# Optimization experiments

Measured on AMD Instinct MI355X. Metric: run time of the kernel, lower is better.

Reference implementation:

```python
import jax, jax.numpy as jnp
import numpy as np
from math import factorial

H = W = 1024
NSC = 4   # n_scales
NOR = 4   # n_orientations
NA = 9


def _grids(h, w):
    # normalized frequency grids, DC at (h//2, w//2) after fftshift
    x = (jnp.arange(w) - w // 2) / (w / 2)
    y = (jnp.arange(h) - h // 2) / (h / 2)
    xr, yr = jnp.meshgrid(x, y, indexing='xy')  # (h, w)
    ang = jnp.arctan2(yr, xr)
    rad = jnp.sqrt(xr * xr + yr * yr)
    rad = rad.at[h // 2, w // 2].set(rad[h // 2, w // 2 - 1])  # avoid log2(0)
    return jnp.log2(rad), ang


def _rc(lr, shift):
    # raised-cosine transition of width 1 (in log2 radius); returns (hi, lo) masks
    t = jnp.clip(lr + shift, 0.0, 1.0)
    return jnp.sin(0.5 * jnp.pi * t), jnp.cos(0.5 * jnp.pi * t)


def _build_pyr(im):
    """Complex steerable pyramid in the frequency domain (downsampled),
    returning (residual highpass, oriented complex bands, residual lowpass,
    unoriented bandpass per scale)."""
    h, w = im.shape
    lr, _ = _grids(h, w)
    hi0m, lo0m = _rc(lr, 1.0)
    imdft = jnp.fft.fftshift(jnp.fft.fft2(im))
    hi0 = jnp.fft.ifft2(jnp.fft.ifftshift(imdft * hi0m)).real
    lodft = imdft * lo0m
    order = NOR - 1
    const = (2.0 ** (2 * order)) * (factorial(order) ** 2) / (NOR * factorial(2 * order))
    bands, unor = [], []
    for s in range(NSC):
        hh, ww = lodft.shape
        lr, ang = _grids(hh, ww)
        him, _ = _rc(lr, 2.0)
        for b in range(NOR):
            th = ang - jnp.pi * b / NOR
            thw = jnp.mod(th + jnp.pi, 2.0 * jnp.pi) - jnp.pi
            am = 2.0 * np.sqrt(const) * (jnp.cos(th) ** order) * (jnp.abs(thw) < jnp.pi / 2)
            bdft = ((-1j) ** order) * lodft * (am * him)
            bands.append(jnp.fft.ifft2(jnp.fft.ifftshift(bdft)))
        unor.append(jnp.fft.ifft2(jnp.fft.ifftshift(lodft * him)).real)
        # downsample lowpass by 2 (crop center of spectrum), apply next lo mask
        lodft = lodft[hh // 4: hh - hh // 4, ww // 4: ww - ww // 4]
        lr2, _ = _grids(hh // 2, ww // 2)
        _, lom = _rc(lr2, 1.0)
        lodft = lodft * lom
    lowpass = jnp.fft.ifft2(jnp.fft.ifftshift(lodft)).real
    return hi0, bands, lowpass, unor


def _autocorr_crop(x, denom, le):
    F = jnp.fft.fft2(x)
    ac = jnp.fft.fftshift(jnp.fft.ifft2(F * jnp.conj(F)).real) / denom
    cx, cy = x.shape[0] // 2, x.shape[1] // 2
    return ac[cx - le: cx + le + 1, cy - le: cy + le + 1]


def _expand(t, f):
    # frequency-domain upsampling by factor f (zero-pad centered spectrum)
    mx, my = t.shape
    T = (f * f) * jnp.fft.fftshift(jnp.fft.fft2(t))
    Te = jnp.zeros((f * mx, f * my), dtype=T.dtype)
    cx, cy = f * mx // 2, f * my // 2
    Te = Te.at[cx - mx // 2: cx + mx // 2, cy - my // 2: cy + my // 2].set(T)
    return jnp.fft.ifft2(jnp.fft.ifftshift(Te))


def _ps_stats(im0):
    S, O, Na = NSC, NOR, NA
    n = im0.size
    mn0, mx0 = jnp.min(im0), jnp.max(im0)
    mean0 = jnp.mean(im0)
    var0 = jnp.sum((im0 - mean0) ** 2) / (n - 1)  # unbiased, like torch.var
    skew0 = jnp.mean((im0 - mean0) ** 3) / var0 ** 1.5
    kurt0 = jnp.mean(jnp.abs(im0 - mean0) ** 4) / var0 ** 2
    statg0 = jnp.stack([mean0, var0, skew0, kurt0, mn0, mx0])

    hi0, bands, lowpass, unor = _build_pyr(im0)
    lowpass = lowpass - jnp.mean(lowpass)
    pyr = [hi0] + bands + [lowpass]
    apyr = [jnp.abs(c) for c in pyr]
    magMeans = jnp.stack([jnp.mean(a) for a in apyr])
    apyr = [a - magMeans[i] for i, a in enumerate(apyr)]

    la = (Na - 1) // 2
    acr = jnp.zeros((Na, Na, S + 1), jnp.float32)
    ace = jnp.zeros((Na, Na, S, O), jnp.float32)
    skew0p = jnp.zeros((S + 1,), jnp.float32)
    kurt0p = jnp.zeros((S + 1,), jnp.float32)

    # ---- lowpass residual: re-filter with height-0 pyramid lowpass (lo0 mask) ----
    ch = lowpass
    le = min(min(ch.shape) // 2 - 1, la)
    lr, _ = _grids(ch.shape[0], ch.shape[1])
    _, lo0m = _rc(lr, 1.0)
    imlp = jnp.fft.ifft2(jnp.fft.ifftshift(jnp.fft.fftshift(jnp.fft.fft2(ch)) * lo0m)).real
    ac = _autocorr_crop(imlp, ch.size, le)
    acr = acr.at[la - le: la + le + 1, la - le: la + le + 1, S].set(ac)
    vari = ac[le, le]
    ok = vari / var0 > 1e-6
    skew0p = skew0p.at[S].set(jnp.where(ok, jnp.mean(imlp ** 3) / vari ** 1.5, 0.0))
    kurt0p = kurt0p.at[S].set(jnp.where(ok, jnp.mean(imlp ** 4) / vari ** 2, 3.0))

    # ---- per-band magnitude autocorr + unoriented band moments ----
    for s in range(S):
        le = la
        for b in range(O):
            chb = apyr[s * O + b + 1]
            le = min(min(chb.shape) // 2 - 1, la)
            ac = _autocorr_crop(chb, chb.size, le)
            ace = ace.at[la - le: la + le + 1, la - le: la + le + 1, s, b].set(ac)
        chu = unor[s]
        # torch stacks (real, zeros): numel doubles, cubic/quartic means halve
        ac = _autocorr_crop(chu, 2 * chu.size, le)
        acr = acr.at[la - le: la + le + 1, la - le: la + le + 1, s].set(ac)
        vari = ac[le, le]
        ok = vari / var0 > 1e-6
        skew0p = skew0p.at[s].set(jnp.where(ok, 0.5 * jnp.mean(chu ** 3) / vari ** 1.5, 0.0))
        kurt0p = kurt0p.at[s].set(jnp.where(ok, 0.5 * jnp.mean(chu ** 4) / vari ** 2, 3.0))

    # ---- cross-orientation / cross-scale correlations ----
    C0 = jnp.zeros((O, O, S + 1), jnp.float32)
    Cx0 = jnp.zeros((O, O, S), jnp.float32)
    Cr0 = jnp.zeros((2 * O, 2 * O, S + 1), jnp.float32)
    Crx0 = jnp.zeros((2 * O, 2 * O, S), jnp.float32)
    for s in range(S):
        csz = pyr[s * O + 1].size
        if s < S - 1:
            pc, rc = [], []
            for b in range(O):
                tmp = _expand(pyr[(s + 1) * O + b + 1], 2) / 4
                r, i = tmp.real, tmp.imag
                mag = jnp.sqrt(r * r + i * i)
                ph = 2.0 * jnp.arctan2(r, i)  # swapped args: faithful to source
                rc.append((mag * jnp.cos(ph), mag * jnp.sin(ph)))
                pc.append(mag)  # |(rt2, it2)| == mag
            parents = jnp.stack([(m - m.mean()).T.ravel() for m in pc], 1)
            rparents = jnp.stack([r.T.ravel() for r, _ in rc] + [i.T.ravel() for _, i in rc], 1)
        else:
            tmp = _expand(lowpass, 2).real / 4
            rparents = jnp.stack([
                tmp.ravel(),
                jnp.roll(tmp, (0, 1), (0, 1)).ravel(),
                jnp.roll(tmp, (0, -1), (0, 1)).ravel(),
                jnp.roll(tmp, (1, 0), (0, 1)).ravel(),
                jnp.roll(tmp, (-1, 0), (0, 1)).ravel()], 1)
            parents = None
        cous = jnp.stack([apyr[s * O + b + 1].T.ravel() for b in range(O)], 1)
        C0 = C0.at[:, :, s].set(cous.T @ cous / csz)
        if parents is not None:
            Cx0 = Cx0.at[:, :, s].set(cous.T @ parents / csz)
        rcous = jnp.stack([pyr[s * O + b + 1].real.T.ravel() for b in range(O)], 1)
        Cr0 = Cr0.at[:O, :O, s].set(rcous.T @ rcous / csz)
        nrp = rparents.shape[1]
        Crx0 = Crx0.at[:O, :nrp, s].set(rcous.T @ rparents / csz)
        if s == S - 1:
            Cr0 = Cr0.at[:nrp, :nrp, S].set(rparents.T @ rparents / (csz / 4))

    vHPR0 = jnp.mean(hi0 ** 2)
    return jnp.concatenate([
        statg0, magMeans, ace.ravel(), skew0p, kurt0p, acr.ravel(),
        C0.ravel(), Cx0.ravel(), Cr0.ravel(), Crx0.ravel(), vHPR0[None]])


def setup_inputs() -> dict:
    key = jax.random.key(0)
    im0 = jax.random.normal(key, (H, W), dtype=jnp.float32)
    return {"im0": im0}


def reference(im0):
    return _ps_stats(im0)
```

## Files before the change

### kernel.cpp

```cpp
#include <hip/hip_runtime.h>

#define PI_F     3.14159265358979323846f
#define TWOPI_F  6.28318530717958647692f
#define HPI_F    1.57079632679489661923f

constexpr int fftT(int N){ return N>=512 ? 256 : (N/2 < 64 ? 64 : N/2); }

#define SL_ACE 340
#define SL_ACR 996
#define SL_ALP 1160
#define SL_TOT 1280
#define REP 8

__device__ __forceinline__ float fcoord(int k, int n){
  int s = k ^ (n>>1);
  return (float)(s - (n>>1)) / (float)(n>>1);
}
__device__ __forceinline__ float lograd(int kr, int kc, int n){
  if (kr==0 && kc==0) return log2f(2.0f/(float)n);
  float x = fcoord(kc,n), y = fcoord(kr,n);
  return 0.5f*log2f(x*x+y*y);
}
__device__ __forceinline__ float rc_sin(float lr, float shift){
  float t = fminf(fmaxf(lr+shift,0.f),1.f); return __sinf(HPI_F*t);
}
__device__ __forceinline__ float rc_cos(float lr, float shift){
  float t = fminf(fmaxf(lr+shift,0.f),1.f); return __cosf(HPI_F*t);
}
__device__ __forceinline__ float cumlo(float lr, int s){
  float cl = rc_cos(lr, 1.f);
  for (int m=1;m<=s;m++) cl *= rc_cos(lr, 1.f-(float)m);
  return cl;
}
__device__ __forceinline__ float bandmask(int kr, int kc, int n, int b){
  float x = fcoord(kc,n), y = fcoord(kr,n);
  float ang = atan2f(y,x);
  float lr = lograd(kr,kc,n);
  float him = rc_sin(lr,2.0f);
  float th = ang - 0.25f*PI_F*(float)b;
  float u = th + PI_F;
  u -= TWOPI_F*floorf(u*(1.0f/TWOPI_F));
  float thw = u - PI_F;
  float c = __cosf(th);
  float am = (fabsf(thw) < HPI_F) ? (1.7888543819998317f*c*c*c) : 0.0f;
  return am*him;
}
__device__ __forceinline__ int lagIdx(int di, int dj){
  if (dj < 0 || (dj==0 && di<0)){ di=-di; dj=-dj; }
  return dj==0 ? 36+di : (dj-1)*9 + (di+4);
}
__device__ __forceinline__ void atomAddD(double* p, double v){
  unsafeAtomicAdd(p, v);
}
template<int NS>
__device__ __forceinline__ void blockAccumN(double* base, const float* vals, float* red){
  const int lane = threadIdx.x & 63, wid = threadIdx.x >> 6;
  const int nw = (int)(blockDim.x >> 6);
  #pragma unroll
  for (int k=0;k<NS;k++){
    float v = vals[k];
    #pragma unroll
    for (int o=32;o>0;o>>=1) v += __shfl_down(v,o);
    if (lane==0) red[k*nw+wid]=v;
  }
  __syncthreads();
  const int rep = (int)((blockIdx.x ^ (blockIdx.y<<1) ^ (blockIdx.z<<2)) & 7) * SL_TOT;
  if ((int)threadIdx.x < NS){
    float s=0.f;
    for (int w2=0;w2<nw;w2++) s += red[(int)threadIdx.x*nw+w2];
    atomAddD(base+rep+(int)threadIdx.x,(double)s);
  }
  __syncthreads();
}

struct ImgD { const float2* src; float2* dst; double* slots; int pre, post, b, ss; float scale; };
struct BArgs { ImgD img[6]; const float* rsrc; const float2* F; const float2* aux; float dirsign; };

#define TWI(k) ((k)+((k)>>4))

template<int N>
__global__ __launch_bounds__(fftT(N)) void k_fftB(BArgs a){
  constexpr int T = fftT(N);
  constexpr int LG = (N==1024)?10:(N==512)?9:(N==256)?8:(N==128)?7:6;
  __shared__ float2 sm[2][N];
  __shared__ float2 tw[N/2 + N/32];
  __shared__ float red[13*4];
  const ImgD d = a.img[blockIdx.y];
  const int row = blockIdx.x, tid = threadIdx.x;
  bool zrow=false;

  for (int k=tid;k<N/2;k+=T){
    float sn,cs; __sincosf(TWOPI_F*(float)k/(float)N,&sn,&cs);
    tw[TWI(k)]=make_float2(cs,sn);
  }

  switch(d.pre){
    case 0: {
      const float2* sp = d.src + (size_t)row*N;
      for (int i=tid;i<N;i+=T) sm[0][i]=sp[i];
    } break;
    case 1: {
      const float* rp = a.rsrc + (size_t)row*N;
      for (int i=tid;i<N;i+=T) sm[0][i]=make_float2(rp[i],0.f);
    } break;
    case 2: {
      const int KC = row + ((row < N/2)? 0 : (1024-N));
      const float2* Fr = a.F + (size_t)KC*1024;
      for (int i=tid;i<N;i+=T){
        int KR = i + ((i < N/2)? 0 : (1024-N));
        float2 v = Fr[KR];
        float lr = lograd(i,row,N);
        float m = cumlo(lr,d.ss)*bandmask(i,row,N,d.b);
        sm[0][i]=make_float2(-v.y*m, v.x*m);
      }
    } break;
    case 3: {
      const int KC = row + ((row < N/2)? 0 : (1024-N));
      const float2* Fr = a.F + (size_t)KC*1024;
      for (int i=tid;i<N;i+=T){
        int KR = i + ((i < N/2)? 0 : (1024-N));
        float2 v = Fr[KR];
        float lr = lograd(i,row,N);
        float m = cumlo(lr,d.ss)*rc_sin(lr,2.f);
        sm[0][i]=make_float2(v.x*m, v.y*m);
      }
    } break;
    case 4: {
      const float2* Fr = a.F + (size_t)row*1024;
      for (int i=tid;i<N;i+=T){
        float2 v = Fr[i];
        float m = rc_sin(lograd(i,row,N),1.f);
        sm[0][i]=make_float2(v.x*m, v.y*m);
      }
    } break;
    case 5: case 6: {
      constexpr int M=N/2, Q=N/4;
      const int fi = (row<Q)? row : (row>=N-Q ? row-M : -1);
      if (fi<0){
        for (int i=tid;i<N;i+=T) sm[0][i]=make_float2(0.f,0.f);
        zrow=true;
      } else {
        const int KC = fi + ((fi < M/2)? 0 : (1024-M));
        const float2* Fr = a.F + (size_t)KC*1024;
        for (int i=tid;i<N;i+=T){
          int fj = (i<Q)? i : (i>=N-Q ? i-M : -1);
          float2 r = make_float2(0.f,0.f);
          if (fj>=0){
            int KR = fj + ((fj < M/2)? 0 : (1024-M));
            float2 v = Fr[KR];
            float lr = lograd(fj,fi,M);
            if (d.pre==5){
              float m = cumlo(lr,d.ss+1)*bandmask(fj,fi,M,d.b);
              r = make_float2(-v.y*m, v.x*m);
            } else {
              if (!(fi==0 && fj==0)){
                float m = cumlo(lr,4);
                r = make_float2(v.x*m, v.y*m);
              }
            }
          }
          sm[0][i]=r;
        }
      }
    } break;
  }

  int cur=0;
  if (!zrow){
    const float ds = a.dirsign;
    for (int ls=0; ls<LG; ++ls){
      const int Ns=1<<ls, sh=LG-1-ls;
      __syncthreads();
      for (int j=tid; j<N/2; j+=T){
        const int m = j & (Ns-1);
        const int base = ((j>>ls)<<(ls+1)) + m;
        float2 va = sm[cur][j];
        float2 vb = sm[cur][j+N/2];
        float2 w = tw[TWI(m<<sh)];
        float wy = ds*w.y;
        float2 bw = make_float2(vb.x*w.x - vb.y*wy, vb.x*wy + vb.y*w.x);
        sm[cur^1][base]    = make_float2(va.x+bw.x, va.y+bw.y);
        sm[cur^1][base+Ns] = make_float2(va.x-bw.x, va.y-bw.y);
      }
      cur ^= 1;
    }
  }
  __syncthreads();

  const float sc = d.scale;
  switch(d.post){
    case 0: {
      float2* dp = d.dst + (size_t)row*N;
      for (int i=tid;i<N;i+=T){ float2 v=sm[cur][i]; dp[i]=make_float2(v.x*sc,v.y*sc); }
    } break;
    case 1: {
      float a1=0.f,a2=0.f;
      for (int i=tid;i<N;i+=T){ float v=sm[cur][i].x*sc; a1+=fabsf(v); a2+=v*v; }
      float vals[2]={a1,a2};
      blockAccumN<2>(d.slots, vals, red);
    } break;
    case 2: {
      float2* dp = d.dst + (size_t)row*N;
      float am=0.f;
      for (int i=tid;i<N;i+=T){
        float2 v=sm[cur][i]; v.x*=sc; v.y*=sc; dp[i]=v;
        am += sqrtf(v.x*v.x+v.y*v.y);
      }
      float vals[1]={am};
      blockAccumN<1>(d.slots, vals, red);
    } break;
    case 3: {
      float2* dp = d.dst + (size_t)row*N;
      float s2=0.f,s3=0.f,s4=0.f;
      for (int i=tid;i<N;i+=T){
        float2 v=sm[cur][i]; v.x*=sc; v.y*=sc; dp[i]=v;
        float x=v.x, x2=x*x; s2+=x2; s3+=x2*x; s4+=x2*x2;
      }
      float vals[3]={s2,s3,s4};
      blockAccumN<3>(d.slots, vals, red);
    } break;
    case 4: {
      const float2* B = a.aux;
      constexpr size_t N2 = (size_t)N*N;
      float acc[13];
      #pragma unroll
      for (int k=0;k<13;k++) acc[k]=0.f;
      for (int i=tid;i<N;i+=T){
        float2 p=sm[cur][i]; p.x*=sc; p.y*=sc;
        float m = sqrtf(p.x*p.x+p.y*p.y);
        float rp=0.f, ip=0.f;
        if (m>0.f){ rp=(p.y*p.y-p.x*p.x)/m; ip=2.f*p.x*p.y/m; }
        size_t pos = (size_t)row*N + i;
        acc[0]+=m;
        #pragma unroll
        for (int k=0;k<4;k++){
          float2 z = B[k*N2+pos];
          float mk = sqrtf(z.x*z.x+z.y*z.y);
          acc[1+k]+=mk*m; acc[5+k]+=z.x*rp; acc[9+k]+=z.x*ip;
        }
      }
      blockAccumN<13>(d.slots, acc, red);
    } break;
  }
}

struct TArgs { float2* base[6]; int n; };
__global__ void k_trip(TArgs t){
  int bi = blockIdx.x, bj = blockIdx.y;
  if (bj < bi) return;
  const int n = t.n;
  float2* img = t.base[blockIdx.z];
  __shared__ float2 t0[32][33], t1[32][33];
  int r0=bi*32, c0=bj*32;
  for (int dy=threadIdx.y; dy<32; dy+=8){
    t0[dy][threadIdx.x] = img[(size_t)(r0+dy)*n + c0 + threadIdx.x];
    if (bi!=bj) t1[dy][threadIdx.x] = img[(size_t)(c0+dy)*n + r0 + threadIdx.x];
  }
  __syncthreads();
  for (int dy=threadIdx.y; dy<32; dy+=8){
    img[(size_t)(c0+dy)*n + r0 + threadIdx.x] = t0[threadIdx.x][dy];
    if (bi!=bj) img[(size_t)(r0+dy)*n + c0 + threadIdx.x] = t1[threadIdx.x][dy];
  }
}

struct AArgs { const float2* base[5]; double* slots[5]; int n, lgn, nmag; };
__global__ __launch_bounds__(256) void k_ac(AArgs a){
  __shared__ float t[72][73];
  __shared__ float red[41*4];
  const int z = blockIdx.z;
  const float2* img = a.base[z];
  const bool mag = z < a.nmag;
  const int n = a.n, lgn = a.lgn;
  const int ty0 = blockIdx.y*64, tx0 = blockIdx.x*64;
  for (int idx = threadIdx.x; idx < 72*72; idx += 256){
    int ly = idx/72, lx = idx-ly*72;
    int gy = (ty0 + ly - 4) & (n-1), gx = (tx0 + lx - 4) & (n-1);
    float2 v = img[((size_t)gy<<lgn) + gx];
    t[ly][lx] = mag ? sqrtf(v.x*v.x+v.y*v.y) : v.x;
  }
  __syncthreads();
  float acc[41];
  #pragma unroll
  for (int k=0;k<41;k++) acc[k]=0.f;
  for (int p = threadIdx.x; p < 4096; p += 256){
    int ly = (p>>6) + 4, lx = (p&63) + 4;
    float m0 = t[ly][lx];
    #pragma unroll
    for (int dj=1; dj<=4; dj++)
      #pragma unroll
      for (int di=-4; di<=4; di++)
        acc[(dj-1)*9 + di+4] += m0 * t[ly+di][lx+dj];
    #pragma unroll
    for (int di=0; di<=4; di++)
      acc[36+di] += m0 * t[ly+di][lx];
  }
  blockAccumN<41>(a.slots[z], acc, red);
}

__global__ void k_init(double* S, float* out, int nout){
  int i = blockIdx.x*blockDim.x + threadIdx.x;
  if (i < REP*SL_TOT) S[i]=0.0;
  if (i < nout) out[i]=0.f;
}
__global__ __launch_bounds__(256) void k_imgstats(const float4* __restrict__ x, float* PB){
  float s1=0.f,s2=0.f,s3=0.f,s4=0.f, mn=3.4e38f, mx=-3.4e38f;
  const int base = blockIdx.x*1024 + threadIdx.x;
  #pragma unroll
  for (int it=0; it<4; ++it){
    float4 v = x[base + it*256];
    float vs[4]={v.x,v.y,v.z,v.w};
    #pragma unroll
    for (int k=0;k<4;k++){
      float t=vs[k], t2=t*t;
      s1+=t; s2+=t2; s3+=t2*t; s4+=t2*t2;
      mn=fminf(mn,t); mx=fmaxf(mx,t);
    }
  }
  __shared__ float wr[6][4];
  int lane=threadIdx.x&63, wid=threadIdx.x>>6;
  float sums[4]={s1,s2,s3,s4};
  #pragma unroll
  for (int k=0;k<4;k++){
    float v=sums[k];
    for (int o=32;o>0;o>>=1) v+=__shfl_down(v,o);
    if (lane==0) wr[k][wid]=v;
  }
  { float v=mn; for (int o=32;o>0;o>>=1) v=fminf(v,__shfl_down(v,o)); if(lane==0) wr[4][wid]=v; }
  { float v=mx; for (int o=32;o>0;o>>=1) v=fmaxf(v,__shfl_down(v,o)); if(lane==0) wr[5][wid]=v; }
  __syncthreads();
  if (threadIdx.x<4)  PB[blockIdx.x*8+threadIdx.x] = wr[threadIdx.x][0]+wr[threadIdx.x][1]+wr[threadIdx.x][2]+wr[threadIdx.x][3];
  if (threadIdx.x==4) PB[blockIdx.x*8+4] = fminf(fminf(wr[4][0],wr[4][1]),fminf(wr[4][2],wr[4][3]));
  if (threadIdx.x==5) PB[blockIdx.x*8+5] = fmaxf(fmaxf(wr[5][0],wr[5][1]),fmaxf(wr[5][2],wr[5][3]));
}
__global__ void k_gram(const float2* __restrict__ B, int n2, double* slots){
  float p[20];
  #pragma unroll
  for (int i=0;i<20;i++) p[i]=0.f;
  int stride = gridDim.x*blockDim.x;
  for (int i=blockIdx.x*blockDim.x+threadIdx.x; i<n2; i+=stride){
    float2 z0=B[i], z1=B[i+(size_t)n2], z2=B[i+2*(size_t)n2], z3=B[i+3*(size_t)n2];
    float m0=sqrtf(z0.x*z0.x+z0.y*z0.y), m1=sqrtf(z1.x*z1.x+z1.y*z1.y);
    float m2=sqrtf(z2.x*z2.x+z2.y*z2.y), m3=sqrtf(z3.x*z3.x+z3.y*z3.y);
    float r0=z0.x, r1=z1.x, r2=z2.x, r3=z3.x;
    p[0]+=m0*m0; p[1]+=m0*m1; p[2]+=m0*m2; p[3]+=m0*m3;
    p[4]+=m1*m1; p[5]+=m1*m2; p[6]+=m1*m3;
    p[7]+=m2*m2; p[8]+=m2*m3; p[9]+=m3*m3;
    p[10]+=r0*r0; p[11]+=r0*r1; p[12]+=r0*r2; p[13]+=r0*r3;
    p[14]+=r1*r1; p[15]+=r1*r2; p[16]+=r1*r3;
    p[17]+=r2*r2; p[18]+=r2*r3; p[19]+=r3*r3;
  }
  __shared__ float red[20*4];
  blockAccumN<20>(slots,p,red);
}
__global__ void k_crx3(const float2* __restrict__ RP, const float2* __restrict__ B3, double* S){
  float a[35];
  #pragma unroll
  for (int i=0;i<35;i++) a[i]=0.f;
  int stride = gridDim.x*blockDim.x;
  for (int idx=blockIdx.x*blockDim.x+threadIdx.x; idx<16384; idx+=stride){
    int u=idx>>7, v=idx&127;
    float P0=RP[idx].x;
    float P1=RP[(u<<7) | ((v-1)&127)].x;
    float P2=RP[(u<<7) | ((v+1)&127)].x;
    float P3=RP[(((u-1)&127)<<7) | v].x;
    float P4=RP[(((u+1)&127)<<7) | v].x;
    float P[5]={P0,P1,P2,P3,P4};
    float R[4];
    #pragma unroll
    for (int b=0;b<4;b++) R[b]=B3[b*16384 + (v<<7) + u].x;
    #pragma unroll
    for (int i=0;i<4;i++)
      #pragma unroll
      for (int j=0;j<5;j++) a[i*5+j]+=R[i]*P[j];
    int k=20;
    #pragma unroll
    for (int i=0;i<5;i++)
      #pragma unroll
      for (int j=i;j<5;j++){ a[k]+=P[i]*P[j]; k++; }
  }
  __shared__ float red[35*4];
  float lo[20], hi[15];
  #pragma unroll
  for (int k=0;k<20;k++) lo[k]=a[k];
  #pragma unroll
  for (int k=0;k<15;k++) hi[k]=a[20+k];
  blockAccumN<20>(S+280, lo, red);
  blockAccumN<15>(S+300, hi, red);
}

template<int LG>
__device__ void ifft2_lds(float* re, float* im, const float2* tw, int S){
  constexpr int N=1<<LG, H=N>>1;
  const int tid=threadIdx.x, T=256;
  for (int ls=LG-1; ls>=0; --ls){
    const int h=1<<ls;
    __syncthreads();
    for (int t=tid; t<N*H; t+=T){
      int r=t>>(LG-1), j=t&(H-1);
      int m=j&(h-1);
      int i0=r*S + ((j>>ls)<<(ls+1)) + m, i1=i0+h;
      float ar=re[i0], ai=im[i0], br=re[i1], bi=im[i1];
      re[i0]=ar+br; im[i0]=ai+bi;
      float dr=ar-br, di=ai-bi;
      float2 w=tw[m<<(LG-1-ls)];
      re[i1]=dr*w.x - di*w.y;
      im[i1]=dr*w.y + di*w.x;
    }
  }
  __syncthreads();
  for (int t=tid;t<N*N;t+=T){
    int r=t>>LG, j=t&(N-1);
    int jb=(int)(__brev((unsigned)j)>>(32-LG));
    if (j<jb){
      int p=r*S+j, q=r*S+jb;
      float x=re[p]; re[p]=re[q]; re[q]=x;
      x=im[p]; im[p]=im[q]; im[q]=x;
    }
  }
  for (int ls=LG-1; ls>=0; --ls){
    const int h=1<<ls;
    __syncthreads();
    for (int t=tid; t<N*H; t+=T){
      int c=t>>(LG-1), j=t&(H-1);
      int m=j&(h-1);
      int i0=(((j>>ls)<<(ls+1))+m)*S + c, i1=i0+h*S;
      float ar=re[i0], ai=im[i0], br=re[i1], bi=im[i1];
      re[i0]=ar+br; im[i0]=ai+bi;
      float dr=ar-br, di=ai-bi;
      float2 w=tw[m<<(LG-1-ls)];
      re[i1]=dr*w.x - di*w.y;
      im[i1]=dr*w.y + di*w.x;
    }
  }
  __syncthreads();
  for (int t=tid;t<N*N;t+=T){
    int c=t>>LG, j=t&(N-1);
    int jb=(int)(__brev((unsigned)j)>>(32-LG));
    if (j<jb){
      int p=j*S+c, q=jb*S+c;
      float x=re[p]; re[p]=re[q]; re[q]=x;
      x=im[p]; im[p]=im[q]; im[q]=x;
    }
  }
  __syncthreads();
}

__global__ __launch_bounds__(256) void k_tail64(const float2* __restrict__ F, double* S){
  __shared__ float re[64*65];
  __shared__ float im[64*65];
  __shared__ float2 tw[32];
  __shared__ float red[41*4];
  __shared__ float shmu;
  const int tid=threadIdx.x;
  const float sc=1.f/4096.f;
  for (int k=tid;k<32;k+=256){
    float sn,cs; __sincosf(TWOPI_F*(float)k/64.f,&sn,&cs);
    tw[k]=make_float2(cs,sn);
  }
  for (int t=tid;t<4096;t+=256){
    int a2=t>>6, b=t&63;
    int KR = b + ((b<32)?0:960);
    int KC = a2 + ((a2<32)?0:960);
    float2 v = F[(size_t)KC*1024+KR];
    float m = cumlo(lograd(b,a2,64),4);
    re[a2*65+b]=v.x*m; im[a2*65+b]=v.y*m;
  }
  ifft2_lds<6>(re,im,tw,65);
  {
    int lane=tid&63, wid=tid>>6;
    float s1=0.f;
    for (int t=tid;t<4096;t+=256) s1 += re[(t>>6)*65+(t&63)];
    float v=s1; for (int o=32;o>0;o>>=1) v+=__shfl_down(v,o);
    if (lane==0) red[wid]=v;
    __syncthreads();
    if (tid==0) shmu=(red[0]+red[1]+red[2]+red[3])*(sc*sc);
    __syncthreads();
    float mu=shmu, adc=0.f;
    for (int t=tid;t<4096;t+=256) adc += fabsf(re[(t>>6)*65+(t&63)]*sc - mu);
    v=adc; for (int o=32;o>0;o>>=1) v+=__shfl_down(v,o);
    if (lane==0) red[wid]=v;
    __syncthreads();
    if (tid==0) S[23]=(double)(red[0]+red[1]+red[2]+red[3]);
    __syncthreads();
  }
  for (int t=tid;t<4096;t+=256){
    int a2=t>>6, b=t&63;
    int KR = b + ((b<32)?0:960);
    int KC = a2 + ((a2<32)?0:960);
    float2 v = F[(size_t)KC*1024+KR];
    float lr = lograd(b,a2,64);
    float m = cumlo(lr,4)*rc_cos(lr,1.f);
    if (t==0) m=0.f;
    re[a2*65+b]=v.x*m; im[a2*65+b]=v.y*m;
  }
  ifft2_lds<6>(re,im,tw,65);
  {
    float s2=0.f,s3=0.f,s4=0.f;
    float acc[41];
    #pragma unroll
    for (int k=0;k<41;k++) acc[k]=0.f;
    for (int p=tid;p<4096;p+=256){
      int y=p>>6, x=p&63;
      float m0u=re[y*65+x];
      float m0=m0u*sc, m02=m0*m0;
      s2+=m02; s3+=m02*m0; s4+=m02*m02;
      #pragma unroll
      for (int dj=1;dj<=4;dj++)
        #pragma unroll
        for (int di=-4;di<=4;di++)
          acc[(dj-1)*9+di+4] += m0u * re[((y+dj)&63)*65 + ((x+di)&63)];
      #pragma unroll
      for (int di=0;di<=4;di++)
        acc[36+di] += m0u * re[y*65 + ((x+di)&63)];
    }
    #pragma unroll
    for (int k=0;k<41;k++) acc[k]*=sc*sc;
    float mom[3]={s2,s3,s4};
    blockAccumN<3>(S+36, mom, red);
    blockAccumN<41>(S+SL_ALP, acc, red);
  }
}

__global__ __launch_bounds__(256) void k_final(const double* __restrict__ S,
                                               const float* __restrict__ PB, float* out){
  __shared__ double SD[SL_TOT];
  __shared__ double sh[6];
  __shared__ double wrD[4][4];
  __shared__ float  wrF[2][4];
  const int tid = threadIdx.x;
  for (int k=tid;k<SL_TOT;k+=256){
    double v=0.0;
    #pragma unroll
    for (int r=0;r<REP;r++) v += S[(size_t)r*SL_TOT+k];
    SD[k]=v;
  }
  {
    int lane=tid&63, wid=tid>>6;
    double p0=PB[tid*8+0], p1=PB[tid*8+1], p2=PB[tid*8+2], p3=PB[tid*8+3];
    float pn=PB[tid*8+4], px=PB[tid*8+5];
    for (int o=32;o>0;o>>=1){ p0+=__shfl_down(p0,o); p1+=__shfl_down(p1,o); p2+=__shfl_down(p2,o); p3+=__shfl_down(p3,o); }
    if (lane==0){ wrD[0][wid]=p0; wrD[1][wid]=p1; wrD[2][wid]=p2; wrD[3][wid]=p3; }
    { float v=pn; for (int o=32;o>0;o>>=1) v=fminf(v,__shfl_down(v,o)); if(lane==0) wrF[0][wid]=v; }
    { float v=px; for (int o=32;o>0;o>>=1) v=fmaxf(v,__shfl_down(v,o)); if(lane==0) wrF[1][wid]=v; }
    __syncthreads();
    if (tid==0){
      for (int k=0;k<4;k++) sh[k]=wrD[k][0]+wrD[k][1]+wrD[k][2]+wrD[k][3];
      sh[4]=(double)fminf(fminf(wrF[0][0],wrF[0][1]),fminf(wrF[0][2],wrF[0][3]));
      sh[5]=(double)fmaxf(fmaxf(wrF[1][0],wrF[1][1]),fmaxf(wrF[1][2],wrF[1][3]));
    }
    __syncthreads();
  }
  const double npix[4]={1048576.0,262144.0,65536.0,16384.0};
  for (int e=tid; e<81*16; e+=256){
    int w=e>>4, s=(e>>2)&3, b=e&3;
    int i=w/9, j=w-i*9;
    int k=lagIdx(i-4,j-4);
    double n2=npix[s];
    double mu=SD[6+s*4+b]/n2;
    out[24+(w*4+s)*4+b]=(float)(SD[SL_ACE+(s*4+b)*41+k]/n2 - mu*mu);
  }
  for (int e=tid; e<81*4; e+=256){
    int w=e>>2, s=e&3;
    int i=w/9, j=w-i*9;
    int k=lagIdx(i-4,j-4);
    out[1330+w*5+s]=(float)(SD[SL_ACR+s*41+k]/(2.0*npix[s]));
  }
  for (int w=tid; w<81; w+=256){
    int i=w/9, j=w-i*9;
    int k=lagIdx(i-4,j-4);
    out[1330+w*5+4]=(float)(SD[SL_ALP+k]/4096.0);
  }
  for (int e=tid; e<64; e+=256){
    int s=e>>4, i=(e>>2)&3, j=e&3;
    int a2=i<j?i:j, bb=i<j?j:i;
    int p=a2*(7-a2)/2+bb;
    double n2=npix[s];
    double Si=SD[6+s*4+i], Sj=SD[6+s*4+j];
    out[1735+(i*4+j)*5+s]=(float)((SD[40+s*20+p]-Si*Sj/n2)/n2);
    out[1879+(i*8+j)*5+s]=(float)(SD[40+s*20+10+p]/n2);
  }
  for (int e=tid; e<48; e+=256){
    int s=e>>4, j=(e>>2)&3, i=e&3;
    double n2=npix[s];
    int pb=120+(s*4+j)*13;
    double Smj=SD[pb];
    double Si=SD[6+s*4+i];
    out[1815+(i*4+j)*4+s]=(float)((SD[pb+1+i]-Si*Smj/n2)/n2);
    out[2199+(i*8+j)*4+s]=(float)(SD[pb+5+i]/n2);
    out[2199+(i*8+(j+4))*4+s]=(float)(SD[pb+9+i]/n2);
  }
  for (int e=tid; e<20; e+=256){
    int i=e/5, j=e%5;
    out[2199+(i*8+j)*4+3]=(float)(SD[280+i*5+j]/16384.0);
  }
  for (int e=tid; e<25; e+=256){
    int i=e/5, j=e%5;
    int a2=i<j?i:j, bb=i<j?j:i;
    int p=a2*(9-a2)/2+bb;
    out[1879+(i*8+j)*5+4]=(float)(SD[300+p]/4096.0);
  }
  if (tid==0){
    const double N0=1048576.0;
    double sum=sh[0], s2=sh[1], s3=sh[2], s4=sh[3];
    double mean0=sum/N0;
    double var0=(s2 - sum*mean0)/(N0-1.0);
    double m3 = s3 - 3.0*mean0*s2 + 2.0*N0*mean0*mean0*mean0;
    double m4 = s4 - 4.0*mean0*s3 + 6.0*mean0*mean0*s2 - 3.0*N0*mean0*mean0*mean0*mean0;
    out[0]=(float)mean0; out[1]=(float)var0;
    out[2]=(float)((m3/N0)/(var0*sqrt(var0)));
    out[3]=(float)((m4/N0)/(var0*var0));
    out[4]=(float)sh[4]; out[5]=(float)sh[5];
    out[6]=(float)(SD[4]/N0);
    for (int s=0;s<4;s++) for (int b=0;b<4;b++) out[7+s*4+b]=(float)(SD[6+s*4+b]/npix[s]);
    out[23]=(float)(SD[23]/4096.0);
    for (int s=0;s<4;s++){
      double n2=npix[s];
      double vari=SD[24+s*3]/(2.0*n2);
      int ok=(vari/var0>1e-6);
      out[1320+s]= ok? (float)(0.5*(SD[25+s*3]/n2)/(vari*sqrt(vari))) : 0.f;
      out[1325+s]= ok? (float)(0.5*(SD[26+s*3]/n2)/(vari*vari)) : 3.f;
    }
    { double vari=SD[36]/4096.0; int ok=(vari/var0>1e-6);
      out[1324]= ok? (float)((SD[37]/4096.0)/(vari*sqrt(vari))) : 0.f;
      out[1329]= ok? (float)((SD[38]/4096.0)/(vari*vari)) : 3.f; }
    out[2455]=(float)(SD[5]/N0);
  }
}

static void launchB(int n, int nimg, const BArgs& a, hipStream_t st){
  switch(n){
    case 1024: k_fftB<1024><<<dim3(1024,nimg),fftT(1024),0,st>>>(a); break;
    case 512:  k_fftB<512 ><<<dim3(512 ,nimg),fftT(512 ),0,st>>>(a); break;
    case 256:  k_fftB<256 ><<<dim3(256 ,nimg),fftT(256 ),0,st>>>(a); break;
    case 128:  k_fftB<128 ><<<dim3(128 ,nimg),fftT(128 ),0,st>>>(a); break;
  }
}

extern "C" void kernel_launch(void* const* d_in, const int* in_sizes, int n_in,
                              void* d_out, int out_size, void* d_ws, size_t ws_size,
                              hipStream_t stream){
  const float* im = (const float*)d_in[0];
  float* out = (float*)d_out;
  char* w = (char*)d_ws;
  float2* F   = (float2*)w;
  float2* CA4 = (float2*)(w + ((size_t)8<<20));
  float2* CC  = (float2*)(w + ((size_t)40<<20));
  float2* CB4 = (float2*)(w + ((size_t)48<<20));
  size_t off = (size_t)64<<20;
  double* S = (double*)(w+off);
  float* PB = (float*)(w+off+(size_t)REP*SL_TOT*8);

  k_init<<<40,256,0,stream>>>(S,out,2456);
  k_imgstats<<<256,256,0,stream>>>((const float4*)im,PB);

  { BArgs a{}; a.rsrc=im; a.dirsign=-1.f;
    a.img[0]=ImgD{nullptr,F,nullptr,1,0,0,0,1.f};
    launchB(1024,1,a,stream); }
  { TArgs t{}; t.base[0]=F; t.n=1024;
    k_trip<<<dim3(32,32,1),dim3(32,8),0,stream>>>(t); }
  { BArgs a{}; a.dirsign=-1.f;
    a.img[0]=ImgD{F,F,nullptr,0,0,0,0,1.f};
    launchB(1024,1,a,stream); }

  for (int s=0;s<4;s++){
    const int n=1024>>s, nt=n/32, n2=n*n, lg=10-s;
    const float inv=1.f/(float)n;
    const int nimg = (s==0)? 6 : 5;
    { BArgs a{}; a.F=F; a.dirsign=1.f;
      for (int b=0;b<4;b++) a.img[b]=ImgD{nullptr,CA4+(size_t)b*n2,nullptr,2,0,b,s,inv};
      a.img[4]=ImgD{nullptr,CC,nullptr,3,0,0,s,inv};
      if (s==0) a.img[5]=ImgD{nullptr,CB4,nullptr,4,0,0,0,inv};
      launchB(n,nimg,a,stream); }
    { TArgs t{}; t.n=n;
      for (int b=0;b<4;b++) t.base[b]=CA4+(size_t)b*n2;
      t.base[4]=CC; if (s==0) t.base[5]=CB4;
      k_trip<<<dim3(nt,nt,nimg),dim3(32,8),0,stream>>>(t); }
    { BArgs a{}; a.dirsign=1.f;
      for (int b=0;b<4;b++) a.img[b]=ImgD{CA4+(size_t)b*n2,CA4+(size_t)b*n2,S+6+s*4+b,0,2,0,0,inv};
      a.img[4]=ImgD{CC,CC,S+24+s*3,0,3,0,0,inv};
      if (s==0) a.img[5]=ImgD{CB4,nullptr,S+4,0,1,0,0,inv};
      launchB(n,nimg,a,stream); }
    k_gram<<<256,256,0,stream>>>(CA4,n2,S+40+s*20);
    { AArgs aa{}; aa.n=n; aa.lgn=lg; aa.nmag=4;
      for (int b=0;b<4;b++){ aa.base[b]=CA4+(size_t)b*n2; aa.slots[b]=S+SL_ACE+(size_t)(s*4+b)*41; }
      aa.base[4]=CC; aa.slots[4]=S+SL_ACR+(size_t)s*41;
      k_ac<<<dim3(n/64,n/64,5),256,0,stream>>>(aa); }
    if (s<3){
      const int nb = (s==0)? 2 : 4;
      for (int b0=0;b0<4;b0+=nb){
        { BArgs a{}; a.F=F; a.dirsign=1.f;
          for (int i=0;i<nb;i++) a.img[i]=ImgD{nullptr,CB4+(size_t)i*n2,nullptr,5,0,b0+i,s,inv};
          launchB(n,nb,a,stream); }
        { TArgs t{}; t.n=n;
          for (int i=0;i<nb;i++) t.base[i]=CB4+(size_t)i*n2;
          k_trip<<<dim3(nt,nt,nb),dim3(32,8),0,stream>>>(t); }
        { BArgs a{}; a.dirsign=1.f; a.aux=CA4;
          for (int i=0;i<nb;i++) a.img[i]=ImgD{CB4+(size_t)i*n2,nullptr,S+120+(size_t)(s*4+b0+i)*13,0,4,0,0,inv};
          launchB(n,nb,a,stream); }
      }
    } else {
      k_tail64<<<1,256,0,stream>>>(F,S);
      { BArgs a{}; a.F=F; a.dirsign=1.f;
        a.img[0]=ImgD{nullptr,CB4,nullptr,6,0,0,4,1.f/128.f};
        launchB(128,1,a,stream); }
      { TArgs t{}; t.base[0]=CB4; t.n=128;
        k_trip<<<dim3(4,4,1),dim3(32,8),0,stream>>>(t); }
      { BArgs a{}; a.dirsign=1.f;
        a.img[0]=ImgD{CB4,CB4,nullptr,0,0,0,0,1.f/128.f};
        launchB(128,1,a,stream); }
      k_crx3<<<64,256,0,stream>>>(CB4,CA4,S);
    }
  }
  k_final<<<1,256,0,stream>>>(S,PB,out);
  (void)in_sizes; (void)n_in; (void)out_size; (void)ws_size;
}
```

Before: 535.1 us.

## Use radix-4 FFT stages, store band magnitudes, and register-tile autocorrelation

The shared-memory FFT now does two radix-2 stages per pass as a radix-4 butterfly, with a final radix-2 stage when the log length is odd. This halves the number of barriers and shared-memory round trips. The band-writing stage now stores the magnitude in place of the imaginary part, so later kernels (gram, cross-products, autocorrelation) read it instead of recomputing sqrt. This assumes no downstream consumer needs the imaginary part. The autocorrelation kernel is rewritten so each thread handles 16 contiguous pixels with float4 shared-memory loads and a padded row stride.

```diff
diff --git a/kernel.cpp b/kernel.cpp
--- a/kernel.cpp
+++ b/kernel.cpp
@@ -168,15 +168,45 @@
   int cur=0;
   if (!zrow){
     const float ds = a.dirsign;
-    for (int ls=0; ls<LG; ++ls){
-      const int Ns=1<<ls, sh=LG-1-ls;
+    int ls2 = 0;
+    for (; ls2+2<=LG; ls2+=2){
+      const int Ns = 1<<ls2;
+      __syncthreads();
+      for (int j=tid; j<N/4; j+=T){
+        const int m = j & (Ns-1);
+        const int base = ((j>>ls2)<<(ls2+2)) + m;
+        float2 x0 = sm[cur][j];
+        float2 x1 = sm[cur][j+N/4];
+        float2 x2 = sm[cur][j+N/2];
+        float2 x3 = sm[cur][j+3*(N/4)];
+        float2 w = tw[TWI(m<<(LG-2-ls2))];
+        float w1x=w.x, w1y=ds*w.y;
+        float w2x = w1x*w1x - w1y*w1y, w2y = 2.f*w1x*w1y;
+        float w3x = w2x*w1x - w2y*w1y, w3y = w2x*w1y + w2y*w1x;
+        float2 b = make_float2(x1.x*w1x - x1.y*w1y, x1.x*w1y + x1.y*w1x);
+        float2 c = make_float2(x2.x*w2x - x2.y*w2y, x2.x*w2y + x2.y*w2x);
+        float2 e = make_float2(x3.x*w3x - x3.y*w3y, x3.x*w3y + x3.y*w3x);
+        float t0x=x0.x+c.x, t0y=x0.y+c.y;
+        float t1x=x0.x-c.x, t1y=x0.y-c.y;
+        float t2x=b.x+e.x,  t2y=b.y+e.y;
+        float t3x=b.x-e.x,  t3y=b.y-e.y;
+        float rtx=-ds*t3y,  rty=ds*t3x;
+        sm[cur^1][base]          = make_float2(t0x+t2x, t0y+t2y);
+        sm[cur^1][base+Ns]       = make_float2(t1x+rtx, t1y+rty);
+        sm[cur^1][base+2*Ns]     = make_float2(t0x-t2x, t0y-t2y);
+        sm[cur^1][base+3*Ns]     = make_float2(t1x-rtx, t1y-rty);
+      }
+      cur ^= 1;
+    }
+    if (LG & 1){
+      const int ls = LG-1, Ns = 1<<ls;
       __syncthreads();
       for (int j=tid; j<N/2; j+=T){
         const int m = j & (Ns-1);
         const int base = ((j>>ls)<<(ls+1)) + m;
         float2 va = sm[cur][j];
         float2 vb = sm[cur][j+N/2];
-        float2 w = tw[TWI(m<<sh)];
+        float2 w = tw[TWI(m)];
         float wy = ds*w.y;
         float2 bw = make_float2(vb.x*w.x - vb.y*wy, vb.x*wy + vb.y*w.x);
         sm[cur^1][base]    = make_float2(va.x+bw.x, va.y+bw.y);
@@ -203,8 +233,10 @@
       float2* dp = d.dst + (size_t)row*N;
       float am=0.f;
       for (int i=tid;i<N;i+=T){
-        float2 v=sm[cur][i]; v.x*=sc; v.y*=sc; dp[i]=v;
-        am += sqrtf(v.x*v.x+v.y*v.y);
+        float2 v=sm[cur][i]; v.x*=sc; v.y*=sc;
+        float m = sqrtf(v.x*v.x+v.y*v.y);
+        dp[i]=make_float2(v.x, m);
+        am += m;
       }
       float vals[1]={am};
       blockAccumN<1>(d.slots, vals, red);
@@ -235,8 +267,7 @@
         #pragma unroll
         for (int k=0;k<4;k++){
           float2 z = B[k*N2+pos];
-          float mk = sqrtf(z.x*z.x+z.y*z.y);
-          acc[1+k]+=mk*m; acc[5+k]+=z.x*rp; acc[9+k]+=z.x*ip;
+          acc[1+k]+=z.y*m; acc[5+k]+=z.x*rp; acc[9+k]+=z.x*ip;
         }
       }
       blockAccumN<13>(d.slots, acc, red);
@@ -265,7 +296,7 @@
 
 struct AArgs { const float2* base[5]; double* slots[5]; int n, lgn, nmag; };
 __global__ __launch_bounds__(256) void k_ac(AArgs a){
-  __shared__ float t[72][73];
+  __shared__ float t[72][76];
   __shared__ float red[41*4];
   const int z = blockIdx.z;
   const float2* img = a.base[z];
@@ -276,23 +307,37 @@
     int ly = idx/72, lx = idx-ly*72;
     int gy = (ty0 + ly - 4) & (n-1), gx = (tx0 + lx - 4) & (n-1);
     float2 v = img[((size_t)gy<<lgn) + gx];
-    t[ly][lx] = mag ? sqrtf(v.x*v.x+v.y*v.y) : v.x;
+    t[ly][lx] = mag ? v.y : v.x;
   }
   __syncthreads();
   float acc[41];
   #pragma unroll
   for (int k=0;k<41;k++) acc[k]=0.f;
-  for (int p = threadIdx.x; p < 4096; p += 256){
-    int ly = (p>>6) + 4, lx = (p&63) + 4;
-    float m0 = t[ly][lx];
-    #pragma unroll
-    for (int dj=1; dj<=4; dj++)
+  const int y  = (threadIdx.x>>2) + 4;
+  const int x0 = (threadIdx.x&3)*16 + 4;
+  float4 m0v[4];
+  #pragma unroll
+  for (int k=0;k<4;k++) m0v[k] = *(const float4*)&t[y][x0+k*4];
+  float* m0 = (float*)m0v;
+  #pragma unroll
+  for (int di=-4; di<=4; ++di){
+    float4 rv[5];
+    #pragma unroll
+    for (int k=0;k<5;k++) rv[k] = *(const float4*)&t[y+di][x0+k*4];
+    float* r = (float*)rv;
+    if (di>=0){
+      float s=0.f;
       #pragma unroll
-      for (int di=-4; di<=4; di++)
-        acc[(dj-1)*9 + di+4] += m0 * t[ly+di][lx+dj];
-    #pragma unroll
-    for (int di=0; di<=4; di++)
-      acc[36+di] += m0 * t[ly+di][lx];
+      for (int k=0;k<16;k++) s += m0[k]*r[k];
+      acc[36+di]+=s;
+    }
+    #pragma unroll
+    for (int dj=1;dj<=4;dj++){
+      float s=0.f;
+      #pragma unroll
+      for (int k=0;k<16;k++) s += m0[k]*r[k+dj];
+      acc[(dj-1)*9+di+4]+=s;
+    }
   }
   blockAccumN<41>(a.slots[z], acc, red);
 }
@@ -339,8 +384,7 @@
   int stride = gridDim.x*blockDim.x;
   for (int i=blockIdx.x*blockDim.x+threadIdx.x; i<n2; i+=stride){
     float2 z0=B[i], z1=B[i+(size_t)n2], z2=B[i+2*(size_t)n2], z3=B[i+3*(size_t)n2];
-    float m0=sqrtf(z0.x*z0.x+z0.y*z0.y), m1=sqrtf(z1.x*z1.x+z1.y*z1.y);
-    float m2=sqrtf(z2.x*z2.x+z2.y*z2.y), m3=sqrtf(z3.x*z3.x+z3.y*z3.y);
+    float m0=z0.y, m1=z1.y, m2=z2.y, m3=z3.y;
     float r0=z0.x, r1=z1.x, r2=z2.x, r3=z3.x;
     p[0]+=m0*m0; p[1]+=m0*m1; p[2]+=m0*m2; p[3]+=m0*m3;
     p[4]+=m1*m1; p[5]+=m1*m2; p[6]+=m1*m3;
```

After: 489.6 us. -8.5%, faster.
